# Performance work log

Measured on AMD Instinct MI355X. Metric: run time of the kernel, lower is better.

The kernel has to match this reference:

```python
import jax, jax.numpy as jnp
import numpy as np

T, B, HW, C_IN, NA, HID = 64, 64, 42, 4, 12, 256
FEAT = 288  # 32 channels * 3 * 3 spatial after 4 stride-2 convs


def setup_inputs() -> dict:
    key = jax.random.key(0)
    ks = jax.random.split(key, 16)
    g = lambda k, s, sc=0.1: jax.random.normal(k, s, jnp.float32) * sc
    z = lambda s: jnp.zeros(s, jnp.float32)
    return {
        "frame": jax.random.uniform(ks[0], (T, B, HW, HW, C_IN), jnp.float32),
        "done": jax.random.bernoulli(ks[1], 0.05, (T, B)),
        "h0": z((2, B, HID)),
        "c0": z((2, B, HID)),
        "conv_w1": g(ks[2], (32, C_IN, 3, 3)), "conv_b1": z((32,)),
        "conv_w2": g(ks[3], (32, 32, 3, 3)), "conv_b2": z((32,)),
        "conv_w3": g(ks[4], (32, 32, 3, 3)), "conv_b3": z((32,)),
        "conv_w4": g(ks[5], (32, 32, 3, 3)), "conv_b4": z((32,)),
        "w_ih0": g(ks[6], (4 * HID, FEAT)), "w_hh0": g(ks[7], (4 * HID, HID)),
        "b_ih0": z((4 * HID,)), "b_hh0": z((4 * HID,)),
        "w_ih1": g(ks[8], (4 * HID, HID)), "w_hh1": g(ks[9], (4 * HID, HID)),
        "b_ih1": z((4 * HID,)), "b_hh1": z((4 * HID,)),
        "policy_w": g(ks[10], (NA, HID)), "policy_b": z((NA,)),
        "baseline_w": g(ks[11], (1, HID)), "baseline_b": z((1,)),
    }


def _lstm_step(x, h, c, w_ih, w_hh, b_ih, b_hh):
    # PyTorch LSTM gate order: i, f, g, o
    gates = x @ w_ih.T + h @ w_hh.T + b_ih + b_hh
    i, f, g, o = jnp.split(gates, 4, axis=-1)
    c_new = jax.nn.sigmoid(f) * c + jax.nn.sigmoid(i) * jnp.tanh(g)
    h_new = jax.nn.sigmoid(o) * jnp.tanh(c_new)
    return h_new, c_new


def reference(frame, done, h0, c0,
              conv_w1, conv_b1, conv_w2, conv_b2, conv_w3, conv_b3, conv_w4, conv_b4,
              w_ih0, w_hh0, b_ih0, b_hh0, w_ih1, w_hh1, b_ih1, b_hh1,
              policy_w, policy_b, baseline_w, baseline_b):
    T_, B_ = frame.shape[:2]
    # torch: view(T,B,W,H,C) [relabel only] -> flatten -> transpose(1,3) == permute(0,3,2,1)
    x = frame.reshape(T_ * B_, HW, HW, C_IN).transpose(0, 3, 2, 1)  # [TB, C, H, W]
    for w, b in ((conv_w1, conv_b1), (conv_w2, conv_b2), (conv_w3, conv_b3), (conv_w4, conv_b4)):
        x = jax.lax.conv_general_dilated(x, w, (2, 2), ((1, 1), (1, 1)),
                                         dimension_numbers=("NCHW", "OIHW", "NCHW"))
        x = jax.nn.elu(x + b[None, :, None, None])
    core_input = x.reshape(T_, B_, FEAT)
    notdone = (~done).astype(jnp.float32)  # [T, B]

    def step(carry, xs):
        h, c = carry           # [2, B, HID] each
        x_t, nd = xs           # [B, FEAT], [B]
        m = nd[None, :, None]
        h, c = h * m, c * m    # reset state where episode ended
        h0n, c0n = _lstm_step(x_t, h[0], c[0], w_ih0, w_hh0, b_ih0, b_hh0)
        h1n, c1n = _lstm_step(h0n, h[1], c[1], w_ih1, w_hh1, b_ih1, b_hh1)
        return (jnp.stack([h0n, h1n]), jnp.stack([c0n, c1n])), h1n

    (hT, cT), outs = jax.lax.scan(step, (h0, c0), (core_input, notdone))
    core_output = outs.reshape(T_ * B_, HID)
    policy_logits = core_output @ policy_w.T + policy_b
    baseline = core_output @ baseline_w.T + baseline_b
    action = jnp.argmax(policy_logits, axis=1)  # eval-mode action
    return (policy_logits.reshape(T_, B_, NA), baseline.reshape(T_, B_),
            action.reshape(T_, B_), hT, cT)
```

## Files before the change

### kernel.cpp

```cpp
#include <hip/hip_runtime.h>
#include <hip/hip_bf16.h>


#define T_ 64
#define B_ 64
#define NTB 4096
#define HID 256
#define G4 1024

typedef float f4 __attribute__((ext_vector_type(4)));

#define XS(j) ((((j) << 2)) ^ ((((j) >> 3) & 7) << 2))

__device__ inline float sigm(float x) { return 1.f / (1.f + __expf(-x)); }
__device__ inline float tanh_(float x) { return 1.f - 2.f / (1.f + __expf(2.f * x)); }
__device__ inline float elu_(float x) { return x > 0.f ? x : __expf(x) - 1.f; }

__global__ void k_prep(const float* __restrict__ wih0, const float* __restrict__ wih1,
                       const float* __restrict__ whh0, const float* __restrict__ whh1,
                       const float* __restrict__ cw2, const float* __restrict__ cw3,
                       const float* __restrict__ cw4, const float* __restrict__ pw,
                       const float* __restrict__ bw,
                       float* __restrict__ wih0T, float* __restrict__ wih1T,
                       float* __restrict__ wq0, float* __restrict__ wq1,
                       float* __restrict__ wc2, float* __restrict__ wc3,
                       float* __restrict__ wc4, float* __restrict__ pwT) {
  int idx = blockIdx.x * 256 + threadIdx.x;
  if (idx < 294912) {
    int k = idx >> 10, j = idx & 1023;
    wih0T[idx] = wih0[j * 288 + k];
  } else if (idx < 557056) {
    int r = idx - 294912; int k = r >> 10, j = r & 1023;
    wih1T[r] = wih1[j * 256 + k];
  } else if (idx < 819200) {
    int r = idx - 557056;
    int cc = r & 3, row = (r >> 2) & 1023, k4 = r >> 12;
    wq0[r] = whh0[row * 256 + k4 * 4 + cc];
  } else if (idx < 1081344) {
    int r = idx - 819200;
    int cc = r & 3, row = (r >> 2) & 1023, k4 = r >> 12;
    wq1[r] = whh1[row * 256 + k4 * 4 + cc];
  } else if (idx < 1108992) {
    int r = idx - 1081344;
    int which = r / 9216; int d = r - which * 9216;
    int i = d & 31, tap = (d >> 5) % 9, o = d / 288;
    int kh = tap / 3, kw = tap - kh * 3;
    const float* src = which == 0 ? cw2 : (which == 1 ? cw3 : cw4);
    float* dst = which == 0 ? wc2 : (which == 1 ? wc3 : wc4);
    dst[d] = src[((o * 32 + i) * 3 + kh) * 3 + kw];
  } else if (idx < 1113088) {
    int r = idx - 1108992; int k = r >> 4, o = r & 15;
    pwT[r] = o < 12 ? pw[o * 256 + k] : (o == 12 ? bw[k] : 0.f);
  }
}

__global__ __launch_bounds__(1024)
void k_donecvt(const unsigned char* __restrict__ db, float* __restrict__ nd) {
  int tid = threadIdx.x;
  const unsigned* dw = (const unsigned*)db;
  unsigned w = dw[tid];
  int odd = ((w & 0xFFFFFF00u) != 0u && w != 0x3F800000u) ? 1 : 0;
  int any = __syncthreads_count(odd);
  bool u8 = (any > 0);
  for (int j = tid; j < 4096; j += 1024) {
    unsigned v = u8 ? (unsigned)db[j] : dw[j];
    nd[j] = v ? 0.f : 1.f;
  }
}

__global__ __launch_bounds__(512, 8)
void k_convall(const float* __restrict__ frame, const float* __restrict__ cw1,
               const float* __restrict__ cb1, const float* __restrict__ wc2,
               const float* __restrict__ cb2, const float* __restrict__ wc3,
               const float* __restrict__ cb3, const float* __restrict__ wc4,
               const float* __restrict__ cb4, float* __restrict__ featT) {
  __shared__ __align__(16) float a1t[8][1792];
  __shared__ __align__(16) float act2l[8][512];
  __shared__ __align__(16) float act3l[8][192];
  int n = blockIdx.x;
  int tid = threadIdx.x;
  const float4* fp = (const float4*)(frame + (size_t)n * 7056);
  int ncol = ((n & 63) << 6) | (n >> 6);

  if (tid < 441) {
    int p = tid / 21, q = tid - (tid / 21) * 21;
    float px[9][4];
#pragma unroll
    for (int kh = 0; kh < 3; ++kh) {
#pragma unroll
      for (int kw = 0; kw < 3; ++kw) {
        int A = 2 * p - 1 + kh, Bc = 2 * q - 1 + kw;
        bool ok = ((unsigned)A < 42u) && ((unsigned)Bc < 42u);
        float4 v = ok ? fp[Bc * 42 + A] : make_float4(0.f, 0.f, 0.f, 0.f);
        px[kh * 3 + kw][0] = v.x; px[kh * 3 + kw][1] = v.y;
        px[kh * 3 + kw][2] = v.z; px[kh * 3 + kw][3] = v.w;
      }
    }
    int col = XS(tid);
#pragma unroll
    for (int oq = 0; oq < 8; ++oq) {
      float4 acc;
      float* ap = (float*)&acc;
#pragma unroll
      for (int j = 0; j < 4; ++j) {
        int o = oq * 4 + j;
        float a = cb1[o];
        const float* w = cw1 + o * 36;
#pragma unroll
        for (int tap = 0; tap < 9; ++tap)
          a += px[tap][0] * w[tap] + px[tap][1] * w[9 + tap] +
               px[tap][2] * w[18 + tap] + px[tap][3] * w[27 + tap];
        ap[j] = elu_(a);
      }
      *(float4*)&a1t[oq][col] = acc;
    }
  }
  __syncthreads();

  {
    int s = tid & 127, oh = tid >> 7;
    int ob = __builtin_amdgcn_readfirstlane(oh << 3);
    if (s < 121) {
      int p = s / 11, q = s - (s / 11) * 11;
      float acc[8];
#pragma unroll
      for (int oi = 0; oi < 8; ++oi) acc[oi] = cb2[ob + oi];
#pragma unroll
      for (int kh = 0; kh < 3; ++kh) {
        int A = 2 * p - 1 + kh;
        if ((unsigned)A >= 21u) continue;
#pragma unroll
        for (int kw = 0; kw < 3; ++kw) {
          int Bc = 2 * q - 1 + kw;
          if ((unsigned)Bc >= 21u) continue;
          int pos = A * 21 + Bc;
          int col = XS(pos);
          int tap = kh * 3 + kw;
#pragma unroll
          for (int i4 = 0; i4 < 8; ++i4) {
            float4 v = *(const float4*)&a1t[i4][col];
#pragma unroll
            for (int oi = 0; oi < 8; ++oi) {
              const float* w = wc2 + ((ob + oi) * 9 + tap) * 32 + i4 * 4;
              acc[oi] += v.x * w[0] + v.y * w[1] + v.z * w[2] + v.w * w[3];
            }
          }
        }
      }
      int colw = XS(s);
#pragma unroll
      for (int half = 0; half < 2; ++half) {
        float4 o4 = make_float4(elu_(acc[half * 4 + 0]), elu_(acc[half * 4 + 1]),
                                elu_(acc[half * 4 + 2]), elu_(acc[half * 4 + 3]));
        *(float4*)&act2l[(ob >> 2) + half][colw] = o4;
      }
    }
  }
  __syncthreads();

  {
    int wv = tid >> 6, lane = tid & 63;
    int oq = __builtin_amdgcn_readfirstlane(wv);
    if (lane < 36) {
      int p = lane / 6, q = lane - (lane / 6) * 6;
      float acc[4];
#pragma unroll
      for (int j = 0; j < 4; ++j) acc[j] = cb3[oq * 4 + j];
#pragma unroll
      for (int kh = 0; kh < 3; ++kh) {
        int A = 2 * p - 1 + kh;
        if ((unsigned)A >= 11u) continue;
#pragma unroll
        for (int kw = 0; kw < 3; ++kw) {
          int Bc = 2 * q - 1 + kw;
          if ((unsigned)Bc >= 11u) continue;
          int col = XS(A * 11 + Bc);
          int tap = kh * 3 + kw;
#pragma unroll
          for (int i4 = 0; i4 < 8; ++i4) {
            float4 v = *(const float4*)&act2l[i4][col];
#pragma unroll
            for (int j = 0; j < 4; ++j) {
              const float* w = wc3 + ((oq * 4 + j) * 9 + tap) * 32 + i4 * 4;
              acc[j] += v.x * w[0] + v.y * w[1] + v.z * w[2] + v.w * w[3];
            }
          }
        }
      }
      float4 o4 = make_float4(elu_(acc[0]), elu_(acc[1]), elu_(acc[2]), elu_(acc[3]));
      *(float4*)&act3l[oq][XS(p * 6 + q)] = o4;
    }
  }
  __syncthreads();

  {
    int wv = tid >> 6, lane = tid & 63;
    int oq = __builtin_amdgcn_readfirstlane(wv);
    if (lane < 9) {
      int p = lane / 3, q = lane - (lane / 3) * 3;
      float acc[4];
#pragma unroll
      for (int j = 0; j < 4; ++j) acc[j] = cb4[oq * 4 + j];
#pragma unroll
      for (int kh = 0; kh < 3; ++kh) {
        int A = 2 * p - 1 + kh;
        if ((unsigned)A >= 6u) continue;
#pragma unroll
        for (int kw = 0; kw < 3; ++kw) {
          int Bc = 2 * q - 1 + kw;
          if ((unsigned)Bc >= 6u) continue;
          int col = XS(A * 6 + Bc);
          int tap = kh * 3 + kw;
#pragma unroll
          for (int i4 = 0; i4 < 8; ++i4) {
            float4 v = *(const float4*)&act3l[i4][col];
#pragma unroll
            for (int j = 0; j < 4; ++j) {
              const float* w = wc4 + ((oq * 4 + j) * 9 + tap) * 32 + i4 * 4;
              acc[j] += v.x * w[0] + v.y * w[1] + v.z * w[2] + v.w * w[3];
            }
          }
        }
      }
#pragma unroll
      for (int j = 0; j < 4; ++j)
        featT[(size_t)((oq * 4 + j) * 9 + lane) * 4096 + ncol] = elu_(acc[j]);
    }
  }
}

__global__ __launch_bounds__(256)
void k_gemm2(const float* __restrict__ inT, const float* __restrict__ wT,
             const float* __restrict__ b1, const float* __restrict__ b2,
             float* __restrict__ out, int K) {
  int nb = blockIdx.x >> 4, jb = blockIdx.x & 15;
  int lane = threadIdx.x & 63, wv = threadIdx.x >> 6;
  int n = nb * 64 + lane;
  int j0 = jb * 64 + __builtin_amdgcn_readfirstlane(wv << 4);
  float acc[16];
#pragma unroll
  for (int m = 0; m < 16; ++m) acc[m] = 0.f;
  const float* ip = inT + n;
#pragma unroll 4
  for (int k = 0; k < K; ++k) {
    float x = ip[(size_t)k * 4096];
    const float* w = wT + k * 1024 + j0;
#pragma unroll
    for (int m = 0; m < 16; ++m) acc[m] += x * w[m];
  }
  float* op = out + (size_t)n * 1024 + j0;
#pragma unroll
  for (int h = 0; h < 4; ++h) {
    float4 o4 = make_float4(acc[h * 4 + 0] + b1[j0 + h * 4 + 0] + b2[j0 + h * 4 + 0],
                            acc[h * 4 + 1] + b1[j0 + h * 4 + 1] + b2[j0 + h * 4 + 1],
                            acc[h * 4 + 2] + b1[j0 + h * 4 + 2] + b2[j0 + h * 4 + 2],
                            acc[h * 4 + 3] + b1[j0 + h * 4 + 3] + b2[j0 + h * 4 + 3]);
    *(float4*)&op[h * 4] = o4;
  }
}

#define WREGS(X) X(0) X(1) X(2) X(3) X(4) X(5) X(6) X(7) \
                 X(8) X(9) X(10) X(11) X(12) X(13) X(14) X(15)

__global__ __launch_bounds__(1024, 4)
void k_scan(const float* __restrict__ wq, const float* __restrict__ G,
            const float* __restrict__ h_init, const float* __restrict__ c_init,
            const float* __restrict__ ndb, float* __restrict__ h_allT,
            float* __restrict__ hT, float* __restrict__ cT) {
  int b = blockIdx.x, j = threadIdx.x;
  __shared__ __align__(16) float hs[256];
  __shared__ __align__(16) f4 wl[8][1024];
  __shared__ float gl[1024];
  __shared__ __align__(16) float hbuf[16][256];
  const f4* wq4 = (const f4*)wq;
#define DECLR(i) f4 wr##i = wq4[(i) * 1024 + j];
  WREGS(DECLR)
#undef DECLR
#pragma unroll
  for (int q = 0; q < 8; ++q) wl[q][j] = wq4[(16 + q) * 1024 + j];
  float c = 0.f;
  if (j < 256) { hs[j] = h_init[b * HID + j]; c = c_init[b * HID + j]; }
  __syncthreads();
  const f4* hs4 = (const f4*)hs;
  const f4* sp = wq4 + 24 * 1024 + j;
  const float* gp = G + (size_t)b * 65536 + j;
  float hlast = 0.f;
  for (int t = 0; t < T_; ++t) {
    float nd = ndb[t * B_ + b];
    f4 acc = {0.f, 0.f, 0.f, 0.f};
#define FMAR(i) { f4 h4 = hs4[i]; acc += h4 * wr##i; }
    WREGS(FMAR)
#undef FMAR
#pragma unroll
    for (int q = 0; q < 8; ++q) { f4 h4 = hs4[16 + q]; acc += h4 * wl[q][j]; }
#pragma unroll 4
    for (int q = 0; q < 40; ++q) { f4 h4 = hs4[24 + q]; acc += h4 * sp[(size_t)q * 1024]; }
    float g = gp[(size_t)t * 1024] + (acc.x + acc.y + acc.z + acc.w) * nd;
    gl[j] = g;
    __syncthreads();
    if (j < 256) {
      float gi = gl[j], gf = gl[j + 256], gg = gl[j + 512], go = gl[j + 768];
      c = sigm(gf) * (c * nd) + sigm(gi) * tanh_(gg);
      float h = sigm(go) * tanh_(c);
      hs[j] = h;
      hbuf[t & 15][j] = h;
      hlast = h;
    }
    __syncthreads();
    if ((t & 15) == 15) {
      int jr = j >> 2, qd = j & 3;
      int t0 = t & ~15;
      float4 o4 = make_float4(hbuf[qd * 4 + 0][jr], hbuf[qd * 4 + 1][jr],
                              hbuf[qd * 4 + 2][jr], hbuf[qd * 4 + 3][jr]);
      *(float4*)&h_allT[(size_t)jr * 4096 + b * 64 + t0 + qd * 4] = o4;
    }
  }
  if (j < 256) { hT[b * HID + j] = hlast; cT[b * HID + j] = c; }
}

__global__ __launch_bounds__(256)
void k_heads(const float* __restrict__ h1aT, const float* __restrict__ pwT,
             const float* __restrict__ pb, const float* __restrict__ bb,
             float* __restrict__ out) {
  int n = blockIdx.x * 256 + threadIdx.x;
  int col = ((n & 63) << 6) | (n >> 6);
  float acc[13];
#pragma unroll
  for (int o = 0; o < 12; ++o) acc[o] = pb[o];
  acc[12] = bb[0];
  for (int k = 0; k < 256; ++k) {
    float h = h1aT[(size_t)k * 4096 + col];
    const float* w = pwT + k * 16;
#pragma unroll
    for (int o = 0; o < 13; ++o) acc[o] += h * w[o];
  }
  float best = acc[0]; int bi = 0;
#pragma unroll
  for (int o = 1; o < 12; ++o)
    if (acc[o] > best) { best = acc[o]; bi = o; }
#pragma unroll
  for (int o = 0; o < 12; ++o) out[n * 12 + o] = acc[o];
  out[49152 + n] = acc[12];
  out[53248 + n] = (float)bi;
}

extern "C" void kernel_launch(void* const* d_in, const int* in_sizes, int n_in,
                              void* d_out, int out_size, void* d_ws, size_t ws_size,
                              hipStream_t stream) {
  const float* frame = (const float*)d_in[0];
  const unsigned char* done = (const unsigned char*)d_in[1];
  const float* h0 = (const float*)d_in[2];
  const float* c0 = (const float*)d_in[3];
  const float* cw1 = (const float*)d_in[4];  const float* cb1 = (const float*)d_in[5];
  const float* cw2 = (const float*)d_in[6];  const float* cb2 = (const float*)d_in[7];
  const float* cw3 = (const float*)d_in[8];  const float* cb3 = (const float*)d_in[9];
  const float* cw4 = (const float*)d_in[10]; const float* cb4 = (const float*)d_in[11];
  const float* wih0 = (const float*)d_in[12]; const float* whh0 = (const float*)d_in[13];
  const float* bih0 = (const float*)d_in[14]; const float* bhh0 = (const float*)d_in[15];
  const float* wih1 = (const float*)d_in[16]; const float* whh1 = (const float*)d_in[17];
  const float* bih1 = (const float*)d_in[18]; const float* bhh1 = (const float*)d_in[19];
  const float* pw = (const float*)d_in[20]; const float* pb = (const float*)d_in[21];
  const float* bw = (const float*)d_in[22]; const float* bb = (const float*)d_in[23];

  float* featT = (float*)d_ws;
  float* G0    = featT + 1179648;
  float* G1    = G0 + 4194304;
  float* h0aT  = G1 + 4194304;
  float* h1aT  = h0aT + 1048576;
  float* wih0T = h1aT + 1048576;
  float* wih1T = wih0T + 294912;
  float* wq0   = wih1T + 262144;
  float* wq1   = wq0 + 262144;
  float* wc2   = wq1 + 262144;
  float* wc3   = wc2 + 9216;
  float* wc4   = wc3 + 9216;
  float* pwT   = wc4 + 9216;
  float* ndb   = pwT + 4096;

  float* out = (float*)d_out;
  float* o_hT = out + 57344;
  float* o_cT = out + 90112;

  k_prep<<<4348, 256, 0, stream>>>(wih0, wih1, whh0, whh1, cw2, cw3, cw4, pw, bw,
                                   wih0T, wih1T, wq0, wq1, wc2, wc3, wc4, pwT);
  k_donecvt<<<1, 1024, 0, stream>>>(done, ndb);
  k_convall<<<4096, 512, 0, stream>>>(frame, cw1, cb1, wc2, cb2, wc3, cb3, wc4, cb4,
                                      featT);
  k_gemm2<<<1024, 256, 0, stream>>>(featT, wih0T, bih0, bhh0, G0, 288);
  k_scan<<<64, 1024, 0, stream>>>(wq0, G0, h0, c0, ndb, h0aT, o_hT, o_cT);
  k_gemm2<<<1024, 256, 0, stream>>>(h0aT, wih1T, bih1, bhh1, G1, 256);
  k_scan<<<64, 1024, 0, stream>>>(wq1, G1, h0 + 16384, c0 + 16384, ndb, h1aT,
                                  o_hT + 16384, o_cT + 16384);
  k_heads<<<16, 256, 0, stream>>>(h1aT, pwT, pb, bb, out);
}
```

Before: 1.712 ms.

## Split LSTM scan across four blocks per batch with global flag barriers

The recurrent scan kernel now uses four 256-thread blocks per batch row instead of one 1024-thread block. Each block computes a quarter of the gate rows, with more weights held in registers and the rest in LDS. Partial gates are written to global memory and the four blocks synchronise every timestep through atomic counters, then each block recomputes the full hidden state redundantly. The aim is to spread the per-step weight matvec over more CUs and cut streaming weight loads. The cost is a global-memory spin barrier and memory fences on every one of the 64 steps, plus deadlock risk if the blocks are not co-resident.

```diff
diff --git a/kernel.cpp b/kernel.cpp
--- a/kernel.cpp
+++ b/kernel.cpp
@@ -259,63 +259,72 @@
   }
 }
 
-#define WREGS(X) X(0) X(1) X(2) X(3) X(4) X(5) X(6) X(7) \
-                 X(8) X(9) X(10) X(11) X(12) X(13) X(14) X(15)
-
-__global__ __launch_bounds__(1024, 4)
-void k_scan(const float* __restrict__ wq, const float* __restrict__ G,
-            const float* __restrict__ h_init, const float* __restrict__ c_init,
-            const float* __restrict__ ndb, float* __restrict__ h_allT,
-            float* __restrict__ hT, float* __restrict__ cT) {
-  int b = blockIdx.x, j = threadIdx.x;
+#define WR48(X) X(0) X(1) X(2) X(3) X(4) X(5) X(6) X(7) X(8) X(9) X(10) X(11) \
+  X(12) X(13) X(14) X(15) X(16) X(17) X(18) X(19) X(20) X(21) X(22) X(23) \
+  X(24) X(25) X(26) X(27) X(28) X(29) X(30) X(31) X(32) X(33) X(34) X(35) \
+  X(36) X(37) X(38) X(39) X(40) X(41) X(42) X(43) X(44) X(45) X(46) X(47)
+
+__global__ __launch_bounds__(256)
+void k_scan4(const float* __restrict__ wq, float* __restrict__ G,
+             const float* __restrict__ h_init, const float* __restrict__ c_init,
+             const float* __restrict__ ndb, int* __restrict__ af,
+             float* __restrict__ h_allT, float* __restrict__ hT,
+             float* __restrict__ cT) {
+  int bid = blockIdx.x;
+  int b = bid & 63, qd = bid >> 6;
+  int tid = threadIdx.x;
+  int r = qd * 256 + tid;
   __shared__ __align__(16) float hs[256];
-  __shared__ __align__(16) f4 wl[8][1024];
-  __shared__ float gl[1024];
-  __shared__ __align__(16) float hbuf[16][256];
+  __shared__ __align__(16) f4 wl[16][256];
+  __shared__ __align__(16) float hbuf[16][64];
   const f4* wq4 = (const f4*)wq;
-#define DECLR(i) f4 wr##i = wq4[(i) * 1024 + j];
-  WREGS(DECLR)
+#define DECLR(i) f4 wr##i = wq4[(i) * 1024 + r];
+  WR48(DECLR)
 #undef DECLR
 #pragma unroll
-  for (int q = 0; q < 8; ++q) wl[q][j] = wq4[(16 + q) * 1024 + j];
-  float c = 0.f;
-  if (j < 256) { hs[j] = h_init[b * HID + j]; c = c_init[b * HID + j]; }
+  for (int q = 0; q < 16; ++q) wl[q][tid] = wq4[(48 + q) * 1024 + r];
+  hs[tid] = h_init[b * HID + tid];
+  float c = c_init[b * HID + tid];
+  float hlast = 0.f;
   __syncthreads();
   const f4* hs4 = (const f4*)hs;
-  const f4* sp = wq4 + 24 * 1024 + j;
-  const float* gp = G + (size_t)b * 65536 + j;
-  float hlast = 0.f;
+  float* gpb = G + (size_t)b * 65536;
+  int* flag = af + b * 64;
   for (int t = 0; t < T_; ++t) {
     float nd = ndb[t * B_ + b];
     f4 acc = {0.f, 0.f, 0.f, 0.f};
 #define FMAR(i) { f4 h4 = hs4[i]; acc += h4 * wr##i; }
-    WREGS(FMAR)
+    WR48(FMAR)
 #undef FMAR
 #pragma unroll
-    for (int q = 0; q < 8; ++q) { f4 h4 = hs4[16 + q]; acc += h4 * wl[q][j]; }
-#pragma unroll 4
-    for (int q = 0; q < 40; ++q) { f4 h4 = hs4[24 + q]; acc += h4 * sp[(size_t)q * 1024]; }
-    float g = gp[(size_t)t * 1024] + (acc.x + acc.y + acc.z + acc.w) * nd;
-    gl[j] = g;
+    for (int q = 0; q < 16; ++q) { f4 h4 = hs4[48 + q]; acc += h4 * wl[q][tid]; }
+    float* grow = gpb + (size_t)t * 1024;
+    float g = grow[r] + (acc.x + acc.y + acc.z + acc.w) * nd;
+    grow[r] = g;
+    __threadfence();
     __syncthreads();
-    if (j < 256) {
-      float gi = gl[j], gf = gl[j + 256], gg = gl[j + 512], go = gl[j + 768];
-      c = sigm(gf) * (c * nd) + sigm(gi) * tanh_(gg);
-      float h = sigm(go) * tanh_(c);
-      hs[j] = h;
-      hbuf[t & 15][j] = h;
-      hlast = h;
-    }
+    if (tid == 0) {
+      atomicAdd(flag + t, 1);
+      while (__hip_atomic_load(flag + t, __ATOMIC_ACQUIRE,
+                               __HIP_MEMORY_SCOPE_AGENT) < 4) {}
+    }
+    __syncthreads();
+    float gi = grow[tid], gf = grow[tid + 256];
+    float gg = grow[tid + 512], go = grow[tid + 768];
+    c = sigm(gf) * (c * nd) + sigm(gi) * tanh_(gg);
+    float h = sigm(go) * tanh_(c);
+    hs[tid] = h;
+    hlast = h;
+    if ((tid >> 6) == qd) hbuf[t & 15][tid & 63] = h;
     __syncthreads();
     if ((t & 15) == 15) {
-      int jr = j >> 2, qd = j & 3;
-      int t0 = t & ~15;
-      float4 o4 = make_float4(hbuf[qd * 4 + 0][jr], hbuf[qd * 4 + 1][jr],
-                              hbuf[qd * 4 + 2][jr], hbuf[qd * 4 + 3][jr]);
-      *(float4*)&h_allT[(size_t)jr * 4096 + b * 64 + t0 + qd * 4] = o4;
-    }
-  }
-  if (j < 256) { hT[b * HID + j] = hlast; cT[b * HID + j] = c; }
+      int jrl = tid >> 2, quad = tid & 3, t0 = t & ~15;
+      float4 o4 = make_float4(hbuf[quad * 4 + 0][jrl], hbuf[quad * 4 + 1][jrl],
+                              hbuf[quad * 4 + 2][jrl], hbuf[quad * 4 + 3][jrl]);
+      *(float4*)&h_allT[(size_t)(qd * 64 + jrl) * 4096 + b * 64 + t0 + quad * 4] = o4;
+    }
+  }
+  if (qd == 0) { hT[b * HID + tid] = hlast; cT[b * HID + tid] = c; }
 }
 
 __global__ __launch_bounds__(256)
@@ -376,20 +385,22 @@
   float* wc4   = wc3 + 9216;
   float* pwT   = wc4 + 9216;
   float* ndb   = pwT + 4096;
+  int*   af    = (int*)(ndb + 4096);
 
   float* out = (float*)d_out;
   float* o_hT = out + 57344;
   float* o_cT = out + 90112;
 
+  hipMemsetAsync(af, 0, 8192 * sizeof(int), stream);
   k_prep<<<4348, 256, 0, stream>>>(wih0, wih1, whh0, whh1, cw2, cw3, cw4, pw, bw,
                                    wih0T, wih1T, wq0, wq1, wc2, wc3, wc4, pwT);
   k_donecvt<<<1, 1024, 0, stream>>>(done, ndb);
   k_convall<<<4096, 512, 0, stream>>>(frame, cw1, cb1, wc2, cb2, wc3, cb3, wc4, cb4,
                                       featT);
   k_gemm2<<<1024, 256, 0, stream>>>(featT, wih0T, bih0, bhh0, G0, 288);
-  k_scan<<<64, 1024, 0, stream>>>(wq0, G0, h0, c0, ndb, h0aT, o_hT, o_cT);
+  k_scan4<<<256, 256, 0, stream>>>(wq0, G0, h0, c0, ndb, af, h0aT, o_hT, o_cT);
   k_gemm2<<<1024, 256, 0, stream>>>(h0aT, wih1T, bih1, bhh1, G1, 256);
-  k_scan<<<64, 1024, 0, stream>>>(wq1, G1, h0 + 16384, c0 + 16384, ndb, h1aT,
-                                  o_hT + 16384, o_cT + 16384);
+  k_scan4<<<256, 256, 0, stream>>>(wq1, G1, h0 + 16384, c0 + 16384, ndb, af + 4096,
+                                   h1aT, o_hT + 16384, o_cT + 16384);
   k_heads<<<16, 256, 0, stream>>>(h1aT, pwT, pb, bb, out);
 }
```

Result: slower. 3.367 ms (+96.6%).
